# Optimization experiments

Hardware: AMD Instinct MI355X
Metric: run time of the kernel (lower is better)

## Reference

```python
import jax, jax.numpy as jnp
import numpy as np

NUM_HEADS = 32
NUM_KV_HEADS = 8
HEAD_DIM = 128
WINDOW = 256
NUM_META = 128
ROPE_BASE = 10000.0


def _rope_cos_sin(seq_len, dim, dtype):
    inv_freq = 1.0 / (ROPE_BASE ** (jnp.arange(0, dim, 2, dtype=jnp.float32) / dim))
    pos = jnp.arange(seq_len, dtype=jnp.float32)
    freqs = pos[:, None] * inv_freq[None, :]          # [S, dim/2]
    emb = jnp.concatenate([freqs, freqs], axis=-1)     # [S, dim]
    return emb.astype(dtype) * 0 + jnp.cos(emb).astype(dtype), jnp.sin(emb).astype(dtype)


def _rotate_half(x):
    x1, x2 = jnp.split(x, 2, axis=-1)
    return jnp.concatenate([-x2, x1], axis=-1)


def setup_inputs() -> dict:
    key = jax.random.key(0)
    k1, k2, k3 = jax.random.split(key, 3)
    B, S = 1, 2176
    return {
        "query_states": jax.random.normal(k1, (B, S, NUM_HEADS * HEAD_DIM), dtype=jnp.float32),
        "key_states": jax.random.normal(k2, (B, S, NUM_KV_HEADS * HEAD_DIM), dtype=jnp.float32),
        "value_states": jax.random.normal(k3, (B, S, NUM_KV_HEADS * HEAD_DIM), dtype=jnp.float32),
    }


def reference(query_states, key_states, value_states):
    B, S, _ = query_states.shape
    n_rep = NUM_HEADS // NUM_KV_HEADS

    q = query_states.reshape(B, S, NUM_HEADS, HEAD_DIM).transpose(0, 2, 1, 3)      # [B,H,S,D]
    k = key_states.reshape(B, S, NUM_KV_HEADS, HEAD_DIM).transpose(0, 2, 1, 3)     # [B,Hk,S,D]
    v = value_states.reshape(B, S, NUM_KV_HEADS, HEAD_DIM).transpose(0, 2, 1, 3)

    # GQA expansion: repeat_interleave along head dim
    k = jnp.repeat(k, n_rep, axis=1)   # [B,H,S,D]
    v = jnp.repeat(v, n_rep, axis=1)

    # inline RoPE on q and (expanded) k
    cos, sin = _rope_cos_sin(S, HEAD_DIM, q.dtype)     # [S,D]
    cos = cos[None, None]
    sin = sin[None, None]
    q = q * cos + _rotate_half(q) * sin
    k = k * cos + _rotate_half(k) * sin

    scale = 1.0 / jnp.sqrt(jnp.asarray(HEAD_DIM, q.dtype))
    scores = jnp.einsum("bhqd,bhkd->bhqk", q, k) * scale

    # mask: causal AND (sliding window OR kv is a prefix meta token)
    q_idx = jnp.arange(S)[:, None]
    kv_idx = jnp.arange(S)[None, :]
    causal = q_idx >= kv_idx
    sliding = (q_idx - kv_idx) <= WINDOW
    prefix = kv_idx < NUM_META
    mask = causal & (sliding | prefix)                 # [S,S]

    scores = jnp.where(mask[None, None], scores, jnp.asarray(-jnp.inf, scores.dtype))
    probs = jax.nn.softmax(scores, axis=-1)
    out = jnp.einsum("bhqk,bhkd->bhqd", probs, v)      # [B,H,S,D]
    return out.transpose(0, 2, 1, 3).reshape(B, S, NUM_HEADS * HEAD_DIM)
```

## Files before the change

kernel.cpp:

```cpp
#include <hip/hip_runtime.h>

#define HQ 32
#define HKV 8
#define DH 128
#define WIN 256
#define META 128
#define QSCALE 0.1275174324f
#define NFREQ 0.20762050594046f

typedef __attribute__((ext_vector_type(8))) __bf16 bf16x8;
typedef __attribute__((ext_vector_type(16))) float f32x16;
typedef __attribute__((ext_vector_type(4))) unsigned int u32x4;
typedef unsigned short u16;
typedef unsigned int u32;

__device__ __forceinline__ u16 f2bf(float f) {
  u32 u = __float_as_uint(f);
  u += 0x7FFFu + ((u >> 16) & 1u);
  return (u16)(u >> 16);
}
__device__ __forceinline__ u32 packbf(float a, float b) {
  u32 ua = __float_as_uint(a); ua += 0x7FFFu + ((ua >> 16) & 1u);
  u32 ub = __float_as_uint(b); ub += 0x7FFFu + ((ub >> 16) & 1u);
  return (ua >> 16) | (ub & 0xFFFF0000u);
}

__global__ __launch_bounds__(256)
void prep_kv(const float* __restrict__ Kg, const float* __restrict__ Vg,
             u16* __restrict__ Kr, u16* __restrict__ Vt, int S) {
  __shared__ float T[64][132];
  const int hk = blockIdx.x;
  const int s0 = blockIdx.y * 64;
  const int tid = threadIdx.x;
  {
    const int r = tid >> 2, c0 = (tid & 3) * 16;
    const int s = s0 + r;
    const float pos = (float)s;
    const float* src = Kg + ((size_t)s * HKV + hk) * DH;
    u16* dst = Kr + ((size_t)hk * S + s) * DH;
    float x[16], y[16];
    #pragma unroll
    for (int j = 0; j < 16; j += 4) {
      *(float4*)&x[j] = *(const float4*)(src + c0 + j);
      *(float4*)&y[j] = *(const float4*)(src + c0 + 64 + j);
    }
    u16 lo[16], hb[16];
    #pragma unroll
    for (int j = 0; j < 16; ++j) {
      float iv = __builtin_amdgcn_exp2f(-NFREQ * (float)(c0 + j));
      float sv, cv; __sincosf(pos * iv, &sv, &cv);
      lo[j] = f2bf(x[j] * cv - y[j] * sv);
      hb[j] = f2bf(y[j] * cv + x[j] * sv);
    }
    *(int4*)(dst + c0)      = *(int4*)&lo[0];
    *(int4*)(dst + c0 + 8)  = *(int4*)&lo[8];
    *(int4*)(dst + c0 + 64) = *(int4*)&hb[0];
    *(int4*)(dst + c0 + 72) = *(int4*)&hb[8];
  }
  {
    const int r = tid >> 2, c = (tid & 3) * 32;
    const float* src = Vg + ((size_t)(s0 + r) * HKV + hk) * DH + c;
    #pragma unroll
    for (int j = 0; j < 32; j += 4) *(float4*)&T[r][c + j] = *(const float4*)(src + j);
  }
  __syncthreads();
  {
    const int d = tid >> 1, hf = (tid & 1) * 32;
    u16 buf[32];
    #pragma unroll
    for (int i = 0; i < 32; ++i) buf[i] = f2bf(T[hf + i][d]);
    u16* dst = Vt + ((size_t)hk * DH + d) * S + s0 + hf;
    #pragma unroll
    for (int j = 0; j < 4; ++j) *(int4*)(dst + j * 8) = *(int4*)&buf[j * 8];
  }
}

#define LOAD_KV(kv0_) do {                                                 \
    const int4* ks_ = (const int4*)(Kb + (size_t)((kv0_) + kr) * DH + kc); \
    fk0 = ks_[0]; fk1 = ks_[1]; fk2 = ks_[2]; fk3 = ks_[3];                \
    const int4* vs_ = (const int4*)(Vb + (kv0_));                          \
    fv0 = vs_[0]; fv1 = vs_[1]; fv2 = vs_[2]; fv3 = vs_[3];                \
  } while (0)

#define STORE_KV() do {                                                    \
    int4* kd_ = (int4*)&Ks[kr][kc];                                        \
    kd_[0] = fk0; kd_[1] = fk1; kd_[2] = fk2; kd_[3] = fk3;                \
    int4* vd_ = (int4*)&Vs[tid >> 1][(tid & 1) * 32];                      \
    vd_[0] = fv0; vd_[1] = fv1; vd_[2] = fv2; vd_[3] = fv3;                \
  } while (0)

__global__ __launch_bounds__(256, 3)
void attn_main(const float* __restrict__ Qg, const u16* __restrict__ Kr,
               const u16* __restrict__ Vt, float* __restrict__ Og, int S) {
  const int h = blockIdx.x;
  const int nqb = gridDim.y;
  const int q0 = (nqb - 1 - blockIdx.y) * 128;
  const int hk = h >> 2;
  const int tid = threadIdx.x;
  const int lane = tid & 63;
  const int wave = tid >> 6;
  const int ln31 = lane & 31;
  const int hi = lane >> 5;
  const int kh = hi * 8;

  __shared__ __align__(16) char smem[35840];
  u16 (*Qs)[136] = (u16(*)[136])smem;
  u16 (*Ks)[136] = (u16(*)[136])smem;
  u16 (*Vs)[72]  = (u16(*)[72])(smem + 17408);

  const u16* Kb = Kr + (size_t)hk * S * DH;
  const u16* Vb = Vt + ((size_t)hk * DH + (tid >> 1)) * S + (tid & 1) * 32;
  const int kr = tid >> 2, kc = (tid & 3) * 32;

  int4 fk0, fk1, fk2, fk3, fv0, fv1, fv2, fv3;
  LOAD_KV(0);

  {
    const int r = tid >> 1, c0 = (tid & 1) * 32;
    const float pos = (float)(q0 + r);
    const float* qrow = Qg + ((size_t)(q0 + r) * HQ + h) * DH;
    #pragma unroll
    for (int c = c0; c < c0 + 32; c += 8) {
      float x[8], y[8];
      *(float4*)&x[0] = *(const float4*)(qrow + c);
      *(float4*)&x[4] = *(const float4*)(qrow + c + 4);
      *(float4*)&y[0] = *(const float4*)(qrow + c + 64);
      *(float4*)&y[4] = *(const float4*)(qrow + c + 68);
      u16 lo[8], hb[8];
      #pragma unroll
      for (int j = 0; j < 8; ++j) {
        float iv = __builtin_amdgcn_exp2f(-NFREQ * (float)(c + j));
        float sv, cv; __sincosf(pos * iv, &sv, &cv);
        lo[j] = f2bf((x[j] * cv - y[j] * sv) * QSCALE);
        hb[j] = f2bf((y[j] * cv + x[j] * sv) * QSCALE);
      }
      __builtin_memcpy(&Qs[r][c], lo, 16);
      __builtin_memcpy(&Qs[r][c + 64], hb, 16);
    }
  }
  __syncthreads();
  const int qw0 = q0 + wave * 32;
  const int q = qw0 + ln31;
  bf16x8 qa[8];
  {
    const u16* qb = &Qs[wave * 32 + ln31][kh];
    #pragma unroll
    for (int kk = 0; kk < 8; ++kk) qa[kk] = *(const bf16x8*)(qb + kk * 16);
  }
  __syncthreads();
  STORE_KV();
  __syncthreads();

  int wstart = q0 - WIN; if (wstart < META) wstart = META;
  int nwin = (q0 + 128 - wstart) >> 6; if (nwin < 0) nwin = 0;
  const int ntiles = 2 + nwin;

  f32x16 acc[4];
  #pragma unroll
  for (int d = 0; d < 4; ++d)
    #pragma unroll
    for (int r = 0; r < 16; ++r) acc[d][r] = 0.f;
  float m_i = -1e30f, l_i = 0.f;

  for (int t = 0; t < ntiles; ++t) {
    const int kv0 = (t < 2) ? t * 64 : wstart + (t - 2) * 64;
    const bool haveNext = (t + 1 < ntiles);
    if (haveNext) {
      const int kvn = (t + 1 < 2) ? (t + 1) * 64 : wstart + (t - 1) * 64;
      LOAD_KV(kvn);
    }

    const bool active = (kv0 <= qw0 + 31) &&
                        ((kv0 < META) || (qw0 - kv0 - 63 <= WIN));
    if (active) {
      f32x16 s0v, s1v;
      #pragma unroll
      for (int r = 0; r < 16; ++r) { s0v[r] = 0.f; s1v[r] = 0.f; }
      const u16* ka0 = &Ks[ln31][kh];
      const u16* ka1 = &Ks[32 + ln31][kh];
      #pragma unroll
      for (int kk = 0; kk < 8; ++kk)
        s0v = __builtin_amdgcn_mfma_f32_32x32x16_bf16(*(const bf16x8*)(ka0 + kk * 16), qa[kk], s0v, 0, 0, 0);
      #pragma unroll
      for (int kk = 0; kk < 8; ++kk)
        s1v = __builtin_amdgcn_mfma_f32_32x32x16_bf16(*(const bf16x8*)(ka1 + kk * 16), qa[kk], s1v, 0, 0, 0);

      const bool fullv = (kv0 + 63 <= qw0) &&
                         ((kv0 + 63 < META) || (qw0 + 31 - kv0 <= WIN));
      if (!fullv) {
        #pragma unroll
        for (int r = 0; r < 16; ++r) {
          const int kva = kv0 + (r & 3) + 8 * (r >> 2) + 4 * hi;
          const int kvb = kva + 32;
          if (!((kva <= q) && (((q - kva) <= WIN) || (kva < META)))) s0v[r] = -1e30f;
          if (!((kvb <= q) && (((q - kvb) <= WIN) || (kvb < META)))) s1v[r] = -1e30f;
        }
      }

      float mx = -1e30f;
      #pragma unroll
      for (int r = 0; r < 16; ++r) mx = fmaxf(mx, fmaxf(s0v[r], s1v[r]));
      mx = fmaxf(mx, __shfl_xor(mx, 32));
      const float mnew = fmaxf(m_i, mx);
      const float al = __builtin_amdgcn_exp2f(m_i - mnew);
      m_i = mnew;
      float ps = 0.f;
      #pragma unroll
      for (int r = 0; r < 16; ++r) {
        s0v[r] = __builtin_amdgcn_exp2f(s0v[r] - mnew);
        s1v[r] = __builtin_amdgcn_exp2f(s1v[r] - mnew);
        ps += s0v[r] + s1v[r];
      }
      ps += __shfl_xor(ps, 32);
      l_i = l_i * al + ps;
      #pragma unroll
      for (int d = 0; d < 4; ++d)
        #pragma unroll
        for (int r = 0; r < 16; ++r) acc[d][r] *= al;

      {
        u32 pk[8], sh[8];
        #pragma unroll
        for (int m = 0; m < 8; ++m) pk[m] = packbf(s0v[2 * m], s0v[2 * m + 1]);
        #pragma unroll
        for (int m = 0; m < 8; ++m) sh[m] = (u32)__shfl_xor((int)pk[m], 32);
        u32x4 bl = { hi ? sh[2] : pk[0], hi ? sh[3] : pk[1],
                     hi ? pk[2] : sh[0], hi ? pk[3] : sh[1] };
        u32x4 bh = { hi ? sh[6] : pk[4], hi ? sh[7] : pk[5],
                     hi ? pk[6] : sh[4], hi ? pk[7] : sh[5] };
        const bf16x8 pbl = __builtin_bit_cast(bf16x8, bl);
        const bf16x8 pbh = __builtin_bit_cast(bf16x8, bh);
        #pragma unroll
        for (int dt = 0; dt < 4; ++dt) {
          const u16* vrow = &Vs[dt * 32 + ln31][kh];
          acc[dt] = __builtin_amdgcn_mfma_f32_32x32x16_bf16(*(const bf16x8*)(vrow),      pbl, acc[dt], 0, 0, 0);
          acc[dt] = __builtin_amdgcn_mfma_f32_32x32x16_bf16(*(const bf16x8*)(vrow + 16), pbh, acc[dt], 0, 0, 0);
        }
      }
      {
        u32 pk[8], sh[8];
        #pragma unroll
        for (int m = 0; m < 8; ++m) pk[m] = packbf(s1v[2 * m], s1v[2 * m + 1]);
        #pragma unroll
        for (int m = 0; m < 8; ++m) sh[m] = (u32)__shfl_xor((int)pk[m], 32);
        u32x4 bl = { hi ? sh[2] : pk[0], hi ? sh[3] : pk[1],
                     hi ? pk[2] : sh[0], hi ? pk[3] : sh[1] };
        u32x4 bh = { hi ? sh[6] : pk[4], hi ? sh[7] : pk[5],
                     hi ? pk[6] : sh[4], hi ? pk[7] : sh[5] };
        const bf16x8 pbl = __builtin_bit_cast(bf16x8, bl);
        const bf16x8 pbh = __builtin_bit_cast(bf16x8, bh);
        #pragma unroll
        for (int dt = 0; dt < 4; ++dt) {
          const u16* vrow = &Vs[dt * 32 + ln31][kh];
          acc[dt] = __builtin_amdgcn_mfma_f32_32x32x16_bf16(*(const bf16x8*)(vrow + 32), pbl, acc[dt], 0, 0, 0);
          acc[dt] = __builtin_amdgcn_mfma_f32_32x32x16_bf16(*(const bf16x8*)(vrow + 48), pbh, acc[dt], 0, 0, 0);
        }
      }
    }

    if (haveNext) {
      __syncthreads();
      STORE_KV();
      __syncthreads();
    }
  }

  const float inv = 1.0f / l_i;
  float* ob = Og + ((size_t)q * HQ + h) * DH;
  #pragma unroll
  for (int dt = 0; dt < 4; ++dt) {
    #pragma unroll
    for (int g = 0; g < 4; ++g) {
      float4 o = { acc[dt][4 * g + 0] * inv, acc[dt][4 * g + 1] * inv,
                   acc[dt][4 * g + 2] * inv, acc[dt][4 * g + 3] * inv };
      *(float4*)(ob + dt * 32 + 8 * g + 4 * hi) = o;
    }
  }
}

extern "C" void kernel_launch(void* const* d_in, const int* in_sizes, int n_in,
                              void* d_out, int out_size, void* d_ws, size_t ws_size,
                              hipStream_t stream) {
  const float* Qg = (const float*)d_in[0];
  const float* Kg = (const float*)d_in[1];
  const float* Vg = (const float*)d_in[2];
  float* Og = (float*)d_out;
  const int S = in_sizes[0] / (HQ * DH);

  u16* Kr = (u16*)d_ws;
  u16* Vt = (u16*)((char*)d_ws + (size_t)HKV * S * DH * 2);

  prep_kv<<<dim3(HKV, S / 64), dim3(256), 0, stream>>>(Kg, Vg, Kr, Vt, S);
  attn_main<<<dim3(HQ, S / 128), dim3(256), 0, stream>>>(Qg, Kr, Vt, Og, S);
}
```

Before: 159.4 us.

## Switch attention to 16x16x32 MFMA with 64-row query blocks and LDS P staging

Halves the query block to 64 rows (16 per wave), which doubles the grid, and replaces the 32x32x16 MFMA tiles with 16x16x32 tiles. The softmax probabilities are now written to a per-wave LDS buffer and reloaded as B operands instead of being shuffled across lanes. The aim is more blocks for occupancy and load balance and simpler P layout handling. The cost is that each K/V tile is now loaded by twice as many blocks, and the LDS footprint grows.

```diff
diff --git a/kernel.cpp b/kernel.cpp
--- a/kernel.cpp
+++ b/kernel.cpp
@@ -9,8 +9,7 @@
 #define NFREQ 0.20762050594046f
 
 typedef __attribute__((ext_vector_type(8))) __bf16 bf16x8;
-typedef __attribute__((ext_vector_type(16))) float f32x16;
-typedef __attribute__((ext_vector_type(4))) unsigned int u32x4;
+typedef __attribute__((ext_vector_type(4))) float f32x4;
 typedef unsigned short u16;
 typedef unsigned int u32;
 
@@ -94,19 +93,20 @@
                const u16* __restrict__ Vt, float* __restrict__ Og, int S) {
   const int h = blockIdx.x;
   const int nqb = gridDim.y;
-  const int q0 = (nqb - 1 - blockIdx.y) * 128;
+  const int q0 = (nqb - 1 - blockIdx.y) * 64;
   const int hk = h >> 2;
   const int tid = threadIdx.x;
   const int lane = tid & 63;
   const int wave = tid >> 6;
-  const int ln31 = lane & 31;
-  const int hi = lane >> 5;
-  const int kh = hi * 8;
-
-  __shared__ __align__(16) char smem[35840];
+  const int qid  = lane & 15;
+  const int quad = lane >> 4;
+  const int k8   = quad * 8;
+
+  __shared__ __align__(16) char smem[45056];
   u16 (*Qs)[136] = (u16(*)[136])smem;
   u16 (*Ks)[136] = (u16(*)[136])smem;
   u16 (*Vs)[72]  = (u16(*)[72])(smem + 17408);
+  u16 (*Ps)[72]  = (u16(*)[72])(smem + 35840);
 
   const u16* Kb = Kr + (size_t)hk * S * DH;
   const u16* Vb = Vt + ((size_t)hk * DH + (tid >> 1)) * S + (tid & 1) * 32;
@@ -116,50 +116,50 @@
   LOAD_KV(0);
 
   {
-    const int r = tid >> 1, c0 = (tid & 1) * 32;
+    const int r = tid >> 2, c0 = (tid & 3) * 16;
     const float pos = (float)(q0 + r);
     const float* qrow = Qg + ((size_t)(q0 + r) * HQ + h) * DH;
-    #pragma unroll
-    for (int c = c0; c < c0 + 32; c += 8) {
-      float x[8], y[8];
-      *(float4*)&x[0] = *(const float4*)(qrow + c);
-      *(float4*)&x[4] = *(const float4*)(qrow + c + 4);
-      *(float4*)&y[0] = *(const float4*)(qrow + c + 64);
-      *(float4*)&y[4] = *(const float4*)(qrow + c + 68);
-      u16 lo[8], hb[8];
-      #pragma unroll
-      for (int j = 0; j < 8; ++j) {
-        float iv = __builtin_amdgcn_exp2f(-NFREQ * (float)(c + j));
-        float sv, cv; __sincosf(pos * iv, &sv, &cv);
-        lo[j] = f2bf((x[j] * cv - y[j] * sv) * QSCALE);
-        hb[j] = f2bf((y[j] * cv + x[j] * sv) * QSCALE);
-      }
-      __builtin_memcpy(&Qs[r][c], lo, 16);
-      __builtin_memcpy(&Qs[r][c + 64], hb, 16);
-    }
-  }
-  __syncthreads();
-  const int qw0 = q0 + wave * 32;
-  const int q = qw0 + ln31;
-  bf16x8 qa[8];
-  {
-    const u16* qb = &Qs[wave * 32 + ln31][kh];
-    #pragma unroll
-    for (int kk = 0; kk < 8; ++kk) qa[kk] = *(const bf16x8*)(qb + kk * 16);
+    float x[16], y[16];
+    #pragma unroll
+    for (int j = 0; j < 16; j += 4) {
+      *(float4*)&x[j] = *(const float4*)(qrow + c0 + j);
+      *(float4*)&y[j] = *(const float4*)(qrow + c0 + 64 + j);
+    }
+    u16 lo[16], hb[16];
+    #pragma unroll
+    for (int j = 0; j < 16; ++j) {
+      float iv = __builtin_amdgcn_exp2f(-NFREQ * (float)(c0 + j));
+      float sv, cv; __sincosf(pos * iv, &sv, &cv);
+      lo[j] = f2bf((x[j] * cv - y[j] * sv) * QSCALE);
+      hb[j] = f2bf((y[j] * cv + x[j] * sv) * QSCALE);
+    }
+    *(int4*)(&Qs[r][c0])      = *(int4*)&lo[0];
+    *(int4*)(&Qs[r][c0 + 8])  = *(int4*)&lo[8];
+    *(int4*)(&Qs[r][c0 + 64]) = *(int4*)&hb[0];
+    *(int4*)(&Qs[r][c0 + 72]) = *(int4*)&hb[8];
+  }
+  __syncthreads();
+  const int qw0 = q0 + wave * 16;
+  const int q   = qw0 + qid;
+  bf16x8 qa[4];
+  {
+    const u16* qb = &Qs[wave * 16 + qid][k8];
+    #pragma unroll
+    for (int c = 0; c < 4; ++c) qa[c] = *(const bf16x8*)(qb + 32 * c);
   }
   __syncthreads();
   STORE_KV();
   __syncthreads();
 
   int wstart = q0 - WIN; if (wstart < META) wstart = META;
-  int nwin = (q0 + 128 - wstart) >> 6; if (nwin < 0) nwin = 0;
+  int nwin = (q0 + 64 - wstart) >> 6; if (nwin < 0) nwin = 0;
   const int ntiles = 2 + nwin;
 
-  f32x16 acc[4];
+  f32x4 acc[8];
   #pragma unroll
-  for (int d = 0; d < 4; ++d)
-    #pragma unroll
-    for (int r = 0; r < 16; ++r) acc[d][r] = 0.f;
+  for (int D = 0; D < 8; ++D)
+    #pragma unroll
+    for (int r = 0; r < 4; ++r) acc[D][r] = 0.f;
   float m_i = -1e30f, l_i = 0.f;
 
   for (int t = 0; t < ntiles; ++t) {
@@ -170,91 +170,77 @@
       LOAD_KV(kvn);
     }
 
-    const bool active = (kv0 <= qw0 + 31) &&
+    const bool active = (kv0 <= qw0 + 15) &&
                         ((kv0 < META) || (qw0 - kv0 - 63 <= WIN));
     if (active) {
-      f32x16 s0v, s1v;
-      #pragma unroll
-      for (int r = 0; r < 16; ++r) { s0v[r] = 0.f; s1v[r] = 0.f; }
-      const u16* ka0 = &Ks[ln31][kh];
-      const u16* ka1 = &Ks[32 + ln31][kh];
-      #pragma unroll
-      for (int kk = 0; kk < 8; ++kk)
-        s0v = __builtin_amdgcn_mfma_f32_32x32x16_bf16(*(const bf16x8*)(ka0 + kk * 16), qa[kk], s0v, 0, 0, 0);
-      #pragma unroll
-      for (int kk = 0; kk < 8; ++kk)
-        s1v = __builtin_amdgcn_mfma_f32_32x32x16_bf16(*(const bf16x8*)(ka1 + kk * 16), qa[kk], s1v, 0, 0, 0);
+      f32x4 sv[4];
+      #pragma unroll
+      for (int T = 0; T < 4; ++T)
+        #pragma unroll
+        for (int r = 0; r < 4; ++r) sv[T][r] = 0.f;
+      #pragma unroll
+      for (int T = 0; T < 4; ++T) {
+        const u16* ka = &Ks[16 * T + qid][k8];
+        #pragma unroll
+        for (int c = 0; c < 4; ++c)
+          sv[T] = __builtin_amdgcn_mfma_f32_16x16x32_bf16(
+                    *(const bf16x8*)(ka + 32 * c), qa[c], sv[T], 0, 0, 0);
+      }
 
       const bool fullv = (kv0 + 63 <= qw0) &&
-                         ((kv0 + 63 < META) || (qw0 + 31 - kv0 <= WIN));
+                         ((kv0 + 63 < META) || (qw0 + 15 - kv0 <= WIN));
       if (!fullv) {
         #pragma unroll
-        for (int r = 0; r < 16; ++r) {
-          const int kva = kv0 + (r & 3) + 8 * (r >> 2) + 4 * hi;
-          const int kvb = kva + 32;
-          if (!((kva <= q) && (((q - kva) <= WIN) || (kva < META)))) s0v[r] = -1e30f;
-          if (!((kvb <= q) && (((q - kvb) <= WIN) || (kvb < META)))) s1v[r] = -1e30f;
+        for (int T = 0; T < 4; ++T) {
+          #pragma unroll
+          for (int r = 0; r < 4; ++r) {
+            const int kv = kv0 + 16 * T + 4 * quad + r;
+            if (!((kv <= q) && (((q - kv) <= WIN) || (kv < META)))) sv[T][r] = -1e30f;
+          }
         }
       }
 
       float mx = -1e30f;
       #pragma unroll
-      for (int r = 0; r < 16; ++r) mx = fmaxf(mx, fmaxf(s0v[r], s1v[r]));
+      for (int T = 0; T < 4; ++T)
+        #pragma unroll
+        for (int r = 0; r < 4; ++r) mx = fmaxf(mx, sv[T][r]);
+      mx = fmaxf(mx, __shfl_xor(mx, 16));
       mx = fmaxf(mx, __shfl_xor(mx, 32));
       const float mnew = fmaxf(m_i, mx);
       const float al = __builtin_amdgcn_exp2f(m_i - mnew);
       m_i = mnew;
       float ps = 0.f;
       #pragma unroll
-      for (int r = 0; r < 16; ++r) {
-        s0v[r] = __builtin_amdgcn_exp2f(s0v[r] - mnew);
-        s1v[r] = __builtin_amdgcn_exp2f(s1v[r] - mnew);
-        ps += s0v[r] + s1v[r];
-      }
-      ps += __shfl_xor(ps, 32);
+      for (int T = 0; T < 4; ++T)
+        #pragma unroll
+        for (int r = 0; r < 4; ++r) {
+          sv[T][r] = __builtin_amdgcn_exp2f(sv[T][r] - mnew);
+          ps += sv[T][r];
+        }
       l_i = l_i * al + ps;
       #pragma unroll
-      for (int d = 0; d < 4; ++d)
-        #pragma unroll
-        for (int r = 0; r < 16; ++r) acc[d][r] *= al;
+      for (int D = 0; D < 8; ++D)
+        #pragma unroll
+        for (int r = 0; r < 4; ++r) acc[D][r] *= al;
 
       {
-        u32 pk[8], sh[8];
-        #pragma unroll
-        for (int m = 0; m < 8; ++m) pk[m] = packbf(s0v[2 * m], s0v[2 * m + 1]);
-        #pragma unroll
-        for (int m = 0; m < 8; ++m) sh[m] = (u32)__shfl_xor((int)pk[m], 32);
-        u32x4 bl = { hi ? sh[2] : pk[0], hi ? sh[3] : pk[1],
-                     hi ? pk[2] : sh[0], hi ? pk[3] : sh[1] };
-        u32x4 bh = { hi ? sh[6] : pk[4], hi ? sh[7] : pk[5],
-                     hi ? pk[6] : sh[4], hi ? pk[7] : sh[5] };
-        const bf16x8 pbl = __builtin_bit_cast(bf16x8, bl);
-        const bf16x8 pbh = __builtin_bit_cast(bf16x8, bh);
-        #pragma unroll
-        for (int dt = 0; dt < 4; ++dt) {
-          const u16* vrow = &Vs[dt * 32 + ln31][kh];
-          acc[dt] = __builtin_amdgcn_mfma_f32_32x32x16_bf16(*(const bf16x8*)(vrow),      pbl, acc[dt], 0, 0, 0);
-          acc[dt] = __builtin_amdgcn_mfma_f32_32x32x16_bf16(*(const bf16x8*)(vrow + 16), pbh, acc[dt], 0, 0, 0);
+        u32* pw = (u32*)&Ps[wave * 16 + qid][0];
+        #pragma unroll
+        for (int T = 0; T < 4; ++T) {
+          pw[8 * T + 2 * quad]     = packbf(sv[T][0], sv[T][1]);
+          pw[8 * T + 2 * quad + 1] = packbf(sv[T][2], sv[T][3]);
         }
       }
-      {
-        u32 pk[8], sh[8];
-        #pragma unroll
-        for (int m = 0; m < 8; ++m) pk[m] = packbf(s1v[2 * m], s1v[2 * m + 1]);
-        #pragma unroll
-        for (int m = 0; m < 8; ++m) sh[m] = (u32)__shfl_xor((int)pk[m], 32);
-        u32x4 bl = { hi ? sh[2] : pk[0], hi ? sh[3] : pk[1],
-                     hi ? pk[2] : sh[0], hi ? pk[3] : sh[1] };
-        u32x4 bh = { hi ? sh[6] : pk[4], hi ? sh[7] : pk[5],
-                     hi ? pk[6] : sh[4], hi ? pk[7] : sh[5] };
-        const bf16x8 pbl = __builtin_bit_cast(bf16x8, bl);
-        const bf16x8 pbh = __builtin_bit_cast(bf16x8, bh);
-        #pragma unroll
-        for (int dt = 0; dt < 4; ++dt) {
-          const u16* vrow = &Vs[dt * 32 + ln31][kh];
-          acc[dt] = __builtin_amdgcn_mfma_f32_32x32x16_bf16(*(const bf16x8*)(vrow + 32), pbl, acc[dt], 0, 0, 0);
-          acc[dt] = __builtin_amdgcn_mfma_f32_32x32x16_bf16(*(const bf16x8*)(vrow + 48), pbh, acc[dt], 0, 0, 0);
-        }
+      const u16* pb = &Ps[wave * 16 + qid][k8];
+      const bf16x8 p0 = *(const bf16x8*)(pb);
+      const bf16x8 p1 = *(const bf16x8*)(pb + 32);
+
+      #pragma unroll
+      for (int D = 0; D < 8; ++D) {
+        const u16* va = &Vs[16 * D + qid][k8];
+        acc[D] = __builtin_amdgcn_mfma_f32_16x16x32_bf16(*(const bf16x8*)(va),      p0, acc[D], 0, 0, 0);
+        acc[D] = __builtin_amdgcn_mfma_f32_16x16x32_bf16(*(const bf16x8*)(va + 32), p1, acc[D], 0, 0, 0);
       }
     }
 
@@ -265,16 +251,14 @@
     }
   }
 
+  l_i += __shfl_xor(l_i, 16);
+  l_i += __shfl_xor(l_i, 32);
   const float inv = 1.0f / l_i;
   float* ob = Og + ((size_t)q * HQ + h) * DH;
   #pragma unroll
-  for (int dt = 0; dt < 4; ++dt) {
-    #pragma unroll
-    for (int g = 0; g < 4; ++g) {
-      float4 o = { acc[dt][4 * g + 0] * inv, acc[dt][4 * g + 1] * inv,
-                   acc[dt][4 * g + 2] * inv, acc[dt][4 * g + 3] * inv };
-      *(float4*)(ob + dt * 32 + 8 * g + 4 * hi) = o;
-    }
+  for (int D = 0; D < 8; ++D) {
+    float4 o = { acc[D][0] * inv, acc[D][1] * inv, acc[D][2] * inv, acc[D][3] * inv };
+    *(float4*)(ob + 16 * D + 4 * quad) = o;
   }
 }
 
@@ -291,5 +275,5 @@
   u16* Vt = (u16*)((char*)d_ws + (size_t)HKV * S * DH * 2);
 
   prep_kv<<<dim3(HKV, S / 64), dim3(256), 0, stream>>>(Kg, Vg, Kr, Vt, S);
-  attn_main<<<dim3(HQ, S / 128), dim3(256), 0, stream>>>(Qg, Kr, Vt, Og, S);
-}
+  attn_main<<<dim3(HQ, S / 64), dim3(256), 0, stream>>>(Qg, Kr, Vt, Og, S);
+}
```

Result: faster. 131.5 us (-17.5%).
